# Kernel tuning notes

Measured on AMD Instinct MI355X. Metric: run time of the kernel, lower is better.

Reference implementation:

```python
import jax, jax.numpy as jnp
import numpy as np

EPS = 1e-5
GROUPS = 32


def conv1x1(x, W, b):
    # x: (B,C,T), W: (O,C), b: (O,)
    return jnp.einsum('bct,oc->bot', x, W) + b[None, :, None]


def group_norm(x, gamma, beta):
    B, C, T = x.shape
    xg = x.reshape(B, GROUPS, (C // GROUPS) * T)
    mu = xg.mean(axis=-1, keepdims=True)
    var = xg.var(axis=-1, keepdims=True)
    xn = ((xg - mu) * jax.lax.rsqrt(var + EPS)).reshape(B, C, T)
    return xn * gamma[None, :, None] + beta[None, :, None]


def block(x, W, b, gamma, beta):
    return jax.nn.relu(group_norm(conv1x1(x, W, b), gamma, beta))


def setup_inputs() -> dict:
    key = jax.random.key(0)
    ks = jax.random.split(key, 8)
    B, C, P, T, TF = 4, 512, 512, 2048, 4096
    inp = {
        'feature': jax.random.normal(ks[0], (B, C, T), jnp.float32),
        'frame_level_feature': jax.random.uniform(ks[1], (B, C, TF), jnp.float32),
        # cur_point_conv: conv1x1 C->P + GN(32,P)
        'W1': jax.random.normal(ks[2], (P, C), jnp.float32) / np.sqrt(C),
        'b1': jnp.zeros((P,), jnp.float32),
        'g1': jnp.ones((P,), jnp.float32),
        'be1': jnp.zeros((P,), jnp.float32),
        # lr_conv: conv1x1 C->2P + GN(32,2P)
        'W2': jax.random.normal(ks[3], (2 * P, C), jnp.float32) / np.sqrt(C),
        'b2': jnp.zeros((2 * P,), jnp.float32),
        'g2': jnp.ones((2 * P,), jnp.float32),
        'be2': jnp.zeros((2 * P,), jnp.float32),
        # proposal_conv: conv1x1 4P->C + GN(32,C)
        'W3': jax.random.normal(ks[4], (C, 4 * P), jnp.float32) / np.sqrt(4 * P),
        'b3': jnp.zeros((C,), jnp.float32),
        'g3': jnp.ones((C,), jnp.float32),
        'be3': jnp.zeros((C,), jnp.float32),
    }
    return inp


def reference(feature, frame_level_feature, W1, b1, g1, be1, W2, b2, g2, be2, W3, b3, g3, be3):
    fm_short = block(feature, W1, b1, g1, be1)          # (B,P,T)
    feat = block(feature, W2, b2, g2, be2)              # (B,2P,T)
    t = feature.shape[2]
    # inverse-CDF resampling (uses batch 0 statistics, as original)
    mean_values = frame_level_feature.mean(axis=1)[0]   # (TF,)
    mean_values = mean_values / mean_values.sum()
    cdf = (jnp.cumsum(mean_values) * t).astype(jnp.int32)
    cdf = jnp.minimum(cdf, t - 1)                       # (TF,)
    # exact vectorization of findNearNum loop: first index with minimal |cdf-i|
    targets = jnp.arange(t, dtype=jnp.int32)
    idx = jnp.argmin(jnp.abs(cdf[None, :] - targets[:, None]), axis=1)  # (t,)
    sampled = frame_level_feature[:, :, idx]            # (B,C,t)
    mixed = jnp.concatenate([sampled, feat, fm_short], axis=1)  # (B,4P,t)
    mixed = block(mixed, W3, b3, g3, be3)               # (B,C,t)
    return (mixed, feat)
```

## Files before the change

kernel.cpp:

```cpp
#include <hip/hip_runtime.h>

typedef unsigned short u16;
typedef unsigned int   u32;
typedef __attribute__((ext_vector_type(8))) short short8;
typedef __attribute__((ext_vector_type(4))) float f32x4;

__device__ __forceinline__ float bf2f(u16 v) {
  return __uint_as_float(((u32)v) << 16);
}
__device__ __forceinline__ u16 f2bf(float f) {
  u32 u = __float_as_uint(f);
  u32 r = (u + 0x7FFFu + ((u >> 16) & 1u)) >> 16;
  return (u16)r;
}
__device__ __forceinline__ float relu(float x) { return x < 0.f ? 0.f : x; }

__device__ __forceinline__ void gld16(const void* g, void* l) {
  __builtin_amdgcn_global_load_lds((const __attribute__((address_space(1))) u32*)g,
                                   (__attribute__((address_space(3))) u32*)l, 16, 0, 0);
}

__global__ void colmean_part_kernel(const float* __restrict__ frame,
                                    double* __restrict__ partD) {
  int tf = blockIdx.x * 256 + threadIdx.x;
  int ch = blockIdx.y;
  const float* f0 = frame + tf + (size_t)ch * 64 * 4096;
  double s = 0.0;
  for (int c = 0; c < 64; ++c) s += (double)f0[(size_t)c * 4096];
  partD[ch * 4096 + tf] = s;
}

__global__ void scanD_kernel(const double* __restrict__ partD, int* __restrict__ cdf) {
  __shared__ double part[256];
  __shared__ double base[256];
  __shared__ double Ss;
  int tid = threadIdx.x;
  double loc[16];
  double s = 0.0;
#pragma unroll
  for (int i = 0; i < 16; ++i) {
    int tf = tid * 16 + i;
    double m = 0.0;
#pragma unroll
    for (int ch = 0; ch < 8; ++ch) m += partD[ch * 4096 + tf];
    loc[i] = m / 512.0;
    s += loc[i];
  }
  part[tid] = s;
  __syncthreads();
  if (tid == 0) {
    double t = 0.0;
    for (int i = 0; i < 256; ++i) t += part[i];
    Ss = t;
  }
  __syncthreads();
  double S = Ss;
  s = 0.0;
#pragma unroll
  for (int i = 0; i < 16; ++i) { loc[i] = loc[i] / S; s += loc[i]; }
  part[tid] = s;
  __syncthreads();
  if (tid == 0) {
    double c = 0.0;
    for (int i = 0; i < 256; ++i) { base[i] = c; c += part[i]; }
  }
  __syncthreads();
  double c = base[tid];
#pragma unroll
  for (int i = 0; i < 16; ++i) {
    c += loc[i];
    int iv = (int)(c * 2048.0);
    cdf[tid * 16 + i] = iv < 2047 ? iv : 2047;
  }
}

__global__ void argmin_kernel(const int* __restrict__ cdf, int* __restrict__ idx) {
  __shared__ int sd[256], sj[256];
  int target = blockIdx.x;
  int tid = threadIdx.x;
  int best = 0x7fffffff, bj = 0x7fffffff;
  for (int j = tid; j < 4096; j += 256) {
    int d = cdf[j] - target; d = d < 0 ? -d : d;
    if (d < best) { best = d; bj = j; }
  }
  sd[tid] = best; sj[tid] = bj;
  __syncthreads();
  for (int s = 128; s > 0; s >>= 1) {
    if (tid < s) {
      if (sd[tid+s] < sd[tid] || (sd[tid+s] == sd[tid] && sj[tid+s] < sj[tid])) {
        sd[tid] = sd[tid+s]; sj[tid] = sj[tid+s];
      }
    }
    __syncthreads();
  }
  if (tid == 0) idx[target] = sj[0];
}

__global__ void gatherT_kernel(const float* __restrict__ frame, const int* __restrict__ idx,
                               u16* __restrict__ X3T) {
  __shared__ u16 tile[64][65];
  __shared__ int sidx[64];
  int cb = blockIdx.x * 64, t0 = blockIdx.y * 64, b = blockIdx.z;
  int tid = threadIdx.x;
  if (tid < 64) {
    int it = idx[t0 + tid];
    sidx[tid] = it < 0 ? 0 : (it > 4095 ? 4095 : it);
  }
  __syncthreads();
  const float* fb = frame + (size_t)b * 512 * 4096;
  for (int i = tid; i < 4096; i += 256) {
    int r = i >> 6, tt = i & 63;
    tile[tt][r] = f2bf(fb[(size_t)(cb + r) * 4096 + sidx[tt]]);
  }
  __syncthreads();
  u16* xb = X3T + (size_t)b * 2048 * 2048;
  for (int i = tid; i < 4096; i += 256) {
    int r = i >> 6, cc = i & 63;
    xb[(size_t)(t0 + r) * 2048 + cb + cc] = tile[r][cc];
  }
}

__global__ void transposeCT_kernel(const float* __restrict__ X, u16* __restrict__ XT) {
  __shared__ u16 tile[64][65];
  int cb = blockIdx.x * 64, t0 = blockIdx.y * 64, b = blockIdx.z;
  int tid = threadIdx.x;
  const float* xb = X + (size_t)b * 512 * 2048;
  for (int i = tid; i < 4096; i += 256) {
    int r = i >> 6, tt = i & 63;
    tile[tt][r] = f2bf(xb[(size_t)(cb + r) * 2048 + t0 + tt]);
  }
  __syncthreads();
  u16* xtb = XT + (size_t)b * 2048 * 512;
  for (int i = tid; i < 4096; i += 256) {
    int r = i >> 6, cc = i & 63;
    xtb[(size_t)(t0 + r) * 512 + cb + cc] = tile[r][cc];
  }
}

__global__ void convW_kernel(const float* __restrict__ src, u16* __restrict__ dst, int n) {
  int i = blockIdx.x * 256 + threadIdx.x;
  if (i < n) dst[i] = f2bf(src[i]);
}

__global__ __launch_bounds__(256) void gemm_bt(
    const u16* __restrict__ A, const u16* __restrict__ Bt,
    const float* __restrict__ bias, float* __restrict__ Y,
    int M, int N, int K)
{
  __shared__ short As[4096];
  __shared__ short Bs[4096];
  const int tid = threadIdx.x;
  const int lane = tid & 63;
  const int w = tid >> 6;
  const int nt = blockIdx.x, mt = blockIdx.y, bb = blockIdx.z;

  const u16* Ab = A + (size_t)mt * 128 * K;
  const u16* Bb = Bt + ((size_t)bb * N + (size_t)nt * 128) * K;

  const int lm = lane & 15, lq = lane >> 4;
  const int wrow = w >> 1, wcol = w & 1;

  f32x4 acc[4][4] = {};

  for (int kt = 0; kt < K; kt += 32) {
    __syncthreads();
#pragma unroll
    for (int p = 0; p < 2; ++p) {
      int q = w + 4 * p;
      int chunk = q * 64 + lane;
      int row = chunk >> 2;
      int ko = (chunk & 3) << 3;
      gld16(Ab + (size_t)row * K + kt + ko, (char*)As + chunk * 16);
      gld16(Bb + (size_t)row * K + kt + ko, (char*)Bs + chunk * 16);
    }
    __syncthreads();
    short8 af[4], bfv[4];
#pragma unroll
    for (int i = 0; i < 4; ++i)
      af[i] = *(const short8*)(As + ((wrow * 64 + i * 16 + lm) * 32 + lq * 8));
#pragma unroll
    for (int j = 0; j < 4; ++j)
      bfv[j] = *(const short8*)(Bs + ((wcol * 64 + j * 16 + lm) * 32 + lq * 8));
#pragma unroll
    for (int i = 0; i < 4; ++i)
#pragma unroll
      for (int j = 0; j < 4; ++j)
        acc[i][j] = __builtin_amdgcn_mfma_f32_16x16x32_bf16(af[i], bfv[j], acc[i][j], 0, 0, 0);
  }

#pragma unroll
  for (int i = 0; i < 4; ++i) {
    int mbase = mt * 128 + wrow * 64 + i * 16 + lq * 4;
#pragma unroll
    for (int e = 0; e < 4; ++e) {
      int m = mbase + e;
      float bv = bias[m];
      float* yp = Y + ((size_t)bb * M + m) * N + nt * 128 + wcol * 64 + lm;
#pragma unroll
      for (int j = 0; j < 4; ++j)
        yp[j * 16] = acc[i][j][e] + bv;
    }
  }
}

__global__ void stats_part_kernel(const float* __restrict__ Y, float* __restrict__ raw,
                                  int C, int cpg) {
  int chunk = blockIdx.x, g = blockIdx.y, b = blockIdx.z, tid = threadIdx.x;
  const float* base = Y + ((size_t)b * C + (size_t)g * cpg) * 2048 + (size_t)chunk * 4096;
  float s = 0.f, ss = 0.f;
#pragma unroll
  for (int i = 0; i < 16; ++i) {
    float v = base[tid + 256 * i];
    s += v; ss += v * v;
  }
  __shared__ float s1[256], s2[256];
  s1[tid] = s; s2[tid] = ss;
  __syncthreads();
  for (int st = 128; st > 0; st >>= 1) {
    if (tid < st) { s1[tid] += s1[tid + st]; s2[tid] += s2[tid + st]; }
    __syncthreads();
  }
  if (tid == 0) {
    atomicAdd(&raw[(b * 32 + g) * 2],     s1[0]);
    atomicAdd(&raw[(b * 32 + g) * 2 + 1], s2[0]);
  }
}

__global__ void stats_fin_kernel(const float* __restrict__ raw, float* __restrict__ stats,
                                 float n) {
  int i = threadIdx.x;
  float mu = raw[i * 2] / n;
  float var = raw[i * 2 + 1] / n - mu * mu;
  stats[i * 2] = mu;
  stats[i * 2 + 1] = 1.0f / sqrtf(var + 1e-5f);
}

__global__ void normT_kernel(const float* __restrict__ Y, const float* __restrict__ stats,
                             const float* __restrict__ gamma, const float* __restrict__ beta,
                             int C, int gShift, u16* __restrict__ X3T, int colBase,
                             float* __restrict__ featOut) {
  __shared__ u16 tile[64][65];
  int b = blockIdx.z, c0 = blockIdx.y * 64, t0 = blockIdx.x * 64;
  const float* yb = Y + (size_t)b * C * 2048;
  for (int i = threadIdx.x; i < 4096; i += 256) {
    int r = i >> 6, cc = i & 63;
    int ch = c0 + r;
    int gI = (b * 32 + (ch >> gShift)) * 2;
    float mu = stats[gI], rs = stats[gI + 1];
    float v = yb[(size_t)ch * 2048 + t0 + cc];
    float o = relu((v - mu) * rs * gamma[ch] + beta[ch]);
    tile[cc][r] = f2bf(o);
    if (featOut) featOut[((size_t)b * C + ch) * 2048 + t0 + cc] = o;
  }
  __syncthreads();
  for (int i = threadIdx.x; i < 4096; i += 256) {
    int r = i >> 6, cc = i & 63;
    X3T[((size_t)b * 2048 + t0 + r) * 2048 + colBase + c0 + cc] = tile[r][cc];
  }
}

__global__ void norm3_kernel(const float* __restrict__ Y, const float* __restrict__ stats,
                             const float* __restrict__ gamma, const float* __restrict__ beta,
                             float* __restrict__ out) {
  int i = blockIdx.x * 256 + threadIdx.x;
  int b = i >> 20;
  int ch = (i >> 11) & 511;
  int gI = (b * 32 + (ch >> 4)) * 2;
  float mu = stats[gI], rs = stats[gI + 1];
  out[i] = relu((Y[i] - mu) * rs * gamma[ch] + beta[ch]);
}

extern "C" void kernel_launch(void* const* d_in, const int* in_sizes, int n_in,
                              void* d_out, int out_size, void* d_ws, size_t ws_size,
                              hipStream_t stream) {
  const float* feature = (const float*)d_in[0];
  const float* frame   = (const float*)d_in[1];
  const float* W1 = (const float*)d_in[2];
  const float* b1 = (const float*)d_in[3];
  const float* g1 = (const float*)d_in[4];
  const float* be1 = (const float*)d_in[5];
  const float* W2 = (const float*)d_in[6];
  const float* b2 = (const float*)d_in[7];
  const float* g2 = (const float*)d_in[8];
  const float* be2 = (const float*)d_in[9];
  const float* W3 = (const float*)d_in[10];
  const float* b3 = (const float*)d_in[11];
  const float* g3 = (const float*)d_in[12];
  const float* be3 = (const float*)d_in[13];

  char* ws = (char*)d_ws;
  u16*    X3T   = (u16*)(ws + 0);
  float*  Y1f   = (float*)(ws + 33554432);
  float*  Y2f   = (float*)(ws + 50331648);
  float*  Y3f   = Y1f;
  u16*    featT = (u16*)(ws + 83886080);
  double* partD = (double*)(ws + 50331648);
  u16*    W1b   = (u16*)(ws + 50331648 + 1048576);
  u16*    W2b   = (u16*)(ws + 33554432);
  u16*    W3b   = (u16*)(ws + 50331648);
  int*    cdf   = (int*)(ws + 92307456);
  int*    idx   = (int*)(ws + 92323840);
  float*  raw1  = (float*)(ws + 92340224);
  float*  raw2  = (float*)(ws + 92341248);
  float*  raw3  = (float*)(ws + 92342272);
  float*  st1   = (float*)(ws + 92343296);
  float*  st2   = (float*)(ws + 92344320);
  float*  st3   = (float*)(ws + 92345344);

  float* outMixed = (float*)d_out;
  float* outFeat  = outMixed + (size_t)4 * 512 * 2048;

  hipMemsetAsync(raw1, 0, 3 * 1024, stream);

  colmean_part_kernel<<<dim3(16, 8), 256, 0, stream>>>(frame, partD);
  scanD_kernel<<<1, 256, 0, stream>>>(partD, cdf);
  argmin_kernel<<<2048, 256, 0, stream>>>(cdf, idx);
  gatherT_kernel<<<dim3(8, 32, 4), 256, 0, stream>>>(frame, idx, X3T);
  transposeCT_kernel<<<dim3(8, 32, 4), 256, 0, stream>>>(feature, featT);

  convW_kernel<<<1024, 256, 0, stream>>>(W1, W1b, 262144);
  gemm_bt<<<dim3(16, 4, 4), 256, 0, stream>>>(W1b, featT, b1, Y1f, 512, 2048, 512);
  stats_part_kernel<<<dim3(8, 32, 4), 256, 0, stream>>>(Y1f, raw1, 512, 16);
  stats_fin_kernel<<<1, 128, 0, stream>>>(raw1, st1, 32768.f);
  normT_kernel<<<dim3(32, 8, 4), 256, 0, stream>>>(Y1f, st1, g1, be1, 512, 4,
                                                   X3T, 1536, (float*)nullptr);
  convW_kernel<<<2048, 256, 0, stream>>>(W2, W2b, 524288);
  gemm_bt<<<dim3(16, 8, 4), 256, 0, stream>>>(W2b, featT, b2, Y2f, 1024, 2048, 512);
  stats_part_kernel<<<dim3(16, 32, 4), 256, 0, stream>>>(Y2f, raw2, 1024, 32);
  stats_fin_kernel<<<1, 128, 0, stream>>>(raw2, st2, 65536.f);
  normT_kernel<<<dim3(32, 16, 4), 256, 0, stream>>>(Y2f, st2, g2, be2, 1024, 5,
                                                    X3T, 512, outFeat);
  convW_kernel<<<4096, 256, 0, stream>>>(W3, W3b, 1048576);
  gemm_bt<<<dim3(16, 4, 4), 256, 0, stream>>>(W3b, X3T, b3, Y3f, 512, 2048, 2048);
  stats_part_kernel<<<dim3(8, 32, 4), 256, 0, stream>>>(Y3f, raw3, 512, 16);
  stats_fin_kernel<<<1, 128, 0, stream>>>(raw3, st3, 32768.f);
  norm3_kernel<<<16384, 256, 0, stream>>>(Y3f, st3, g3, be3, outMixed);
}
```

Before: 308.8 us.

## Double-buffer GEMM LDS tiles and shrink block tile to 64x128 with two waves

Replaces the 128x128 four-wave GEMM with a 64x128 two-wave variant that double-buffers the A and B tiles in LDS. Each iteration now needs one barrier instead of two, and the next K-slice prefetch overlaps the MFMA work on the current one. Halving the M tile doubles the number of workgroups, so more CUs are busy on this 256-CU part. The cost is more LDS per block and more redundant B-tile reloads across M tiles.

```diff
diff --git a/kernel.cpp b/kernel.cpp
--- a/kernel.cpp
+++ b/kernel.cpp
@@ -142,45 +142,53 @@
   if (i < n) dst[i] = f2bf(src[i]);
 }
 
-__global__ __launch_bounds__(256) void gemm_bt(
+__global__ __launch_bounds__(128) void gemm_bt2(
     const u16* __restrict__ A, const u16* __restrict__ Bt,
     const float* __restrict__ bias, float* __restrict__ Y,
     int M, int N, int K)
 {
-  __shared__ short As[4096];
-  __shared__ short Bs[4096];
+  __shared__ short As[2][2048];
+  __shared__ short Bs[2][4096];
   const int tid = threadIdx.x;
   const int lane = tid & 63;
   const int w = tid >> 6;
   const int nt = blockIdx.x, mt = blockIdx.y, bb = blockIdx.z;
 
-  const u16* Ab = A + (size_t)mt * 128 * K;
+  const u16* Ab = A + (size_t)mt * 64 * K;
   const u16* Bb = Bt + ((size_t)bb * N + (size_t)nt * 128) * K;
 
   const int lm = lane & 15, lq = lane >> 4;
-  const int wrow = w >> 1, wcol = w & 1;
 
   f32x4 acc[4][4] = {};
-
-  for (int kt = 0; kt < K; kt += 32) {
+  const int nsteps = K >> 5;
+
+  auto stage = [&](int buf, int kt) {
+#pragma unroll
+    for (int p = 0; p < 2; ++p) {
+      int chunk = tid + 128 * p;
+      int row = chunk >> 2, ko = (chunk & 3) << 3;
+      gld16(Ab + (size_t)row * K + kt + ko, (char*)As[buf] + chunk * 16);
+    }
+#pragma unroll
+    for (int p = 0; p < 4; ++p) {
+      int chunk = tid + 128 * p;
+      int row = chunk >> 2, ko = (chunk & 3) << 3;
+      gld16(Bb + (size_t)row * K + kt + ko, (char*)Bs[buf] + chunk * 16);
+    }
+  };
+
+  stage(0, 0);
+  for (int s = 0; s < nsteps; ++s) {
+    int cur = s & 1;
     __syncthreads();
-#pragma unroll
-    for (int p = 0; p < 2; ++p) {
-      int q = w + 4 * p;
-      int chunk = q * 64 + lane;
-      int row = chunk >> 2;
-      int ko = (chunk & 3) << 3;
-      gld16(Ab + (size_t)row * K + kt + ko, (char*)As + chunk * 16);
-      gld16(Bb + (size_t)row * K + kt + ko, (char*)Bs + chunk * 16);
-    }
-    __syncthreads();
+    if (s + 1 < nsteps) stage(cur ^ 1, (s + 1) << 5);
     short8 af[4], bfv[4];
 #pragma unroll
     for (int i = 0; i < 4; ++i)
-      af[i] = *(const short8*)(As + ((wrow * 64 + i * 16 + lm) * 32 + lq * 8));
+      af[i] = *(const short8*)(As[cur] + ((i * 16 + lm) * 32 + lq * 8));
 #pragma unroll
     for (int j = 0; j < 4; ++j)
-      bfv[j] = *(const short8*)(Bs + ((wcol * 64 + j * 16 + lm) * 32 + lq * 8));
+      bfv[j] = *(const short8*)(Bs[cur] + ((w * 64 + j * 16 + lm) * 32 + lq * 8));
 #pragma unroll
     for (int i = 0; i < 4; ++i)
 #pragma unroll
@@ -190,12 +198,12 @@
 
 #pragma unroll
   for (int i = 0; i < 4; ++i) {
-    int mbase = mt * 128 + wrow * 64 + i * 16 + lq * 4;
+    int mbase = mt * 64 + i * 16 + lq * 4;
 #pragma unroll
     for (int e = 0; e < 4; ++e) {
       int m = mbase + e;
       float bv = bias[m];
-      float* yp = Y + ((size_t)bb * M + m) * N + nt * 128 + wcol * 64 + lm;
+      float* yp = Y + ((size_t)bb * M + m) * N + nt * 128 + w * 64 + lm;
 #pragma unroll
       for (int j = 0; j < 4; ++j)
         yp[j * 16] = acc[i][j][e] + bv;
@@ -319,19 +327,19 @@
   transposeCT_kernel<<<dim3(8, 32, 4), 256, 0, stream>>>(feature, featT);
 
   convW_kernel<<<1024, 256, 0, stream>>>(W1, W1b, 262144);
-  gemm_bt<<<dim3(16, 4, 4), 256, 0, stream>>>(W1b, featT, b1, Y1f, 512, 2048, 512);
+  gemm_bt2<<<dim3(16, 8, 4), 128, 0, stream>>>(W1b, featT, b1, Y1f, 512, 2048, 512);
   stats_part_kernel<<<dim3(8, 32, 4), 256, 0, stream>>>(Y1f, raw1, 512, 16);
   stats_fin_kernel<<<1, 128, 0, stream>>>(raw1, st1, 32768.f);
   normT_kernel<<<dim3(32, 8, 4), 256, 0, stream>>>(Y1f, st1, g1, be1, 512, 4,
                                                    X3T, 1536, (float*)nullptr);
   convW_kernel<<<2048, 256, 0, stream>>>(W2, W2b, 524288);
-  gemm_bt<<<dim3(16, 8, 4), 256, 0, stream>>>(W2b, featT, b2, Y2f, 1024, 2048, 512);
+  gemm_bt2<<<dim3(16, 16, 4), 128, 0, stream>>>(W2b, featT, b2, Y2f, 1024, 2048, 512);
   stats_part_kernel<<<dim3(16, 32, 4), 256, 0, stream>>>(Y2f, raw2, 1024, 32);
   stats_fin_kernel<<<1, 128, 0, stream>>>(raw2, st2, 65536.f);
   normT_kernel<<<dim3(32, 16, 4), 256, 0, stream>>>(Y2f, st2, g2, be2, 1024, 5,
                                                     X3T, 512, outFeat);
   convW_kernel<<<4096, 256, 0, stream>>>(W3, W3b, 1048576);
-  gemm_bt<<<dim3(16, 4, 4), 256, 0, stream>>>(W3b, X3T, b3, Y3f, 512, 2048, 2048);
+  gemm_bt2<<<dim3(16, 8, 4), 128, 0, stream>>>(W3b, X3T, b3, Y3f, 512, 2048, 2048);
   stats_part_kernel<<<dim3(8, 32, 4), 256, 0, stream>>>(Y3f, raw3, 512, 16);
   stats_fin_kernel<<<1, 128, 0, stream>>>(raw3, st3, 32768.f);
   norm3_kernel<<<16384, 256, 0, stream>>>(Y3f, st3, g3, be3, outMixed);
```

After: 299.6 us. -3.0%, faster.
